# Kernel tuning notes

Measured on AMD Instinct MI355X. Metric: run time of the kernel, lower is better.

## Reference

```python
import jax, jax.numpy as jnp
import numpy as np

B, L, K, D = 4, 48, 32, 128
EPS = 1e-5


def setup_inputs() -> dict:
    key = jax.random.key(0)
    ks = jax.random.split(key, 12)
    s = 1.0 / np.sqrt(D)
    s2 = 1.0 / np.sqrt(2 * D)
    return {
        "h": jax.random.normal(ks[0], (B, L, K, D), jnp.float32),
        # message_mlp: Linear(D,D) -> ReLU -> Linear(D,D); weights stored (in,out)
        "Wm1": jax.random.normal(ks[1], (D, D), jnp.float32) * s,
        "bm1": jnp.zeros((D,), jnp.float32),
        "Wm2": jax.random.normal(ks[2], (D, D), jnp.float32) * s,
        "bm2": jnp.zeros((D,), jnp.float32),
        # attn_mlp: Linear(2D,D) -> ReLU -> Linear(D,1)
        "Wa1": jax.random.normal(ks[3], (2 * D, D), jnp.float32) * s2,
        "ba1": jnp.zeros((D,), jnp.float32),
        "Wa2": jax.random.normal(ks[4], (D, 1), jnp.float32) * s,
        "ba2": jnp.zeros((1,), jnp.float32),
        # LayerNorm(D)
        "gamma": jnp.ones((D,), jnp.float32),
        "beta": jnp.zeros((D,), jnp.float32),
    }


def reference(h, Wm1, bm1, Wm2, bm2, Wa1, ba1, Wa2, ba2, gamma, beta):
    # messages: (B,L,K,D)
    messages = jax.nn.relu(h @ Wm1 + bm1) @ Wm2 + bm2

    # attn_mlp first layer on cat(h_i, h_j): split Wa1 so we never build the 2D concat
    hi_proj = h @ Wa1[:D]   # (B,L,K,D) contribution from h_i (varies over dim 1)
    hj_proj = h @ Wa1[D:]   # (B,L,K,D) contribution from h_j (varies over dim 2)
    # hidden: (B,L,L,K,D)
    hidden = jax.nn.relu(hi_proj[:, :, None, :, :] + hj_proj[:, None, :, :, :] + ba1)
    # logits: (B,L,L,K)
    attn_logits = jnp.einsum("bijkd,d->bijk", hidden, Wa2[:, 0]) + ba2[0]
    attn_weights = jax.nn.softmax(attn_logits, axis=2)  # softmax over j

    # aggregated[b,i,k,:] = sum_j w[b,i,j,k] * messages[b,j,k,:]
    aggregated = jnp.einsum("bijk,bjkd->bikd", attn_weights, messages)

    x = h + aggregated
    mu = jnp.mean(x, axis=-1, keepdims=True)
    var = jnp.mean(jnp.square(x - mu), axis=-1, keepdims=True)
    return (x - mu) * jax.lax.rsqrt(var + EPS) * gamma + beta
```

## Files before the change

### kernel.cpp

```cpp
#include <hip/hip_runtime.h>
#include <math.h>

#define Bc 4
#define Lc 48
#define Kc 32
#define Dc 128
#define ROWS (Bc*Lc*Kc)
#define RT 48
#define NRT (ROWS/RT)
#define GT 512

static_assert(NRT == 128, "role decode assumes 128 row tiles");

__device__ __forceinline__ void gemm_regs(
    const float* __restrict__ sA, const float* __restrict__ sB,
    int rg, int c0, float acc[3][4])
{
    const float* A0 = sA + rg*3*Dc;
    #pragma unroll 8
    for (int k = 0; k < Dc; k += 4) {
        float4 a0 = *(const float4*)(A0 + k);
        float4 a1 = *(const float4*)(A0 + Dc + k);
        float4 a2 = *(const float4*)(A0 + 2*Dc + k);
        float4 b0 = *(const float4*)(sB + (k+0)*Dc + c0);
        float4 b1 = *(const float4*)(sB + (k+1)*Dc + c0);
        float4 b2 = *(const float4*)(sB + (k+2)*Dc + c0);
        float4 b3 = *(const float4*)(sB + (k+3)*Dc + c0);
        float a_[3][4] = {{a0.x,a0.y,a0.z,a0.w},{a1.x,a1.y,a1.z,a1.w},{a2.x,a2.y,a2.z,a2.w}};
        float b_[4][4] = {{b0.x,b0.y,b0.z,b0.w},{b1.x,b1.y,b1.z,b1.w},
                          {b2.x,b2.y,b2.z,b2.w},{b3.x,b3.y,b3.z,b3.w}};
        #pragma unroll
        for (int r = 0; r < 3; ++r)
            #pragma unroll
            for (int c = 0; c < 4; ++c)
                #pragma unroll
                for (int q = 0; q < 4; ++q)
                    acc[r][c] = fmaf(a_[r][q], b_[q][c], acc[r][c]);
    }
}

__global__ __launch_bounds__(GT) void k_gemm_all(
    const float* __restrict__ h,
    const float* __restrict__ Wm1, const float* __restrict__ bm1,
    const float* __restrict__ Wm2, const float* __restrict__ bm2,
    const float* __restrict__ Wa1, const float* __restrict__ ba1,
    float* __restrict__ msg_ws, float* __restrict__ hip_ws,
    float* __restrict__ hjp_ws)
{
    __shared__ float sA[RT*Dc];
    __shared__ float sT[RT*Dc];
    __shared__ float sB[Dc*Dc];
    __shared__ float sBias[Dc];

    const int tid = threadIdx.x;
    const int sel = blockIdx.x >> 7;
    const int r0  = (blockIdx.x & 127) * RT;

    const float* W1; const float* b1;
    if (sel == 0)      { W1 = Wm1;          b1 = bm1; }
    else if (sel == 1) { W1 = Wa1;          b1 = ba1; }
    else               { W1 = Wa1 + Dc*Dc;  b1 = nullptr; }

    {
        const float4* src = (const float4*)W1;
        float4* dst = (float4*)sB;
        #pragma unroll
        for (int i = 0; i < (Dc*Dc/4)/GT; ++i) dst[tid + i*GT] = src[tid + i*GT];
        const float4* asrc = (const float4*)(h + r0*Dc);
        float4* adst = (float4*)sA;
        #pragma unroll
        for (int i = 0; i < (RT*Dc/4)/GT; ++i) adst[tid + i*GT] = asrc[tid + i*GT];
        if (tid < Dc/4)
            ((float4*)sBias)[tid] = b1 ? ((const float4*)b1)[tid]
                                       : make_float4(0.f, 0.f, 0.f, 0.f);
    }
    __syncthreads();

    const int rg = tid >> 5;
    const int c0 = (tid & 31) * 4;
    float acc[3][4] = {};
    gemm_regs(sA, sB, rg, c0, acc);

    if (sel != 0) {
        float* out = (sel == 1) ? hip_ws : hjp_ws;
        #pragma unroll
        for (int r = 0; r < 3; ++r) {
            float4 v;
            v.x = acc[r][0] + sBias[c0+0];
            v.y = acc[r][1] + sBias[c0+1];
            v.z = acc[r][2] + sBias[c0+2];
            v.w = acc[r][3] + sBias[c0+3];
            *(float4*)(out + (r0 + rg*3 + r)*Dc + c0) = v;
        }
        return;
    }

    #pragma unroll
    for (int r = 0; r < 3; ++r) {
        float4 v;
        v.x = fmaxf(acc[r][0] + sBias[c0+0], 0.f);
        v.y = fmaxf(acc[r][1] + sBias[c0+1], 0.f);
        v.z = fmaxf(acc[r][2] + sBias[c0+2], 0.f);
        v.w = fmaxf(acc[r][3] + sBias[c0+3], 0.f);
        *(float4*)(sT + (rg*3+r)*Dc + c0) = v;
    }
    __syncthreads();

    {
        const float4* src = (const float4*)Wm2;
        float4* dst = (float4*)sB;
        #pragma unroll
        for (int i = 0; i < (Dc*Dc/4)/GT; ++i) dst[tid + i*GT] = src[tid + i*GT];
        if (tid < Dc/4) ((float4*)sBias)[tid] = ((const float4*)bm2)[tid];
    }
    __syncthreads();

    float acc2[3][4] = {};
    gemm_regs(sT, sB, rg, c0, acc2);
    #pragma unroll
    for (int r = 0; r < 3; ++r) {
        float4 v;
        v.x = acc2[r][0] + sBias[c0+0];
        v.y = acc2[r][1] + sBias[c0+1];
        v.z = acc2[r][2] + sBias[c0+2];
        v.w = acc2[r][3] + sBias[c0+3];
        *(float4*)(msg_ws + (r0 + rg*3 + r)*Dc + c0) = v;
    }
}

__global__ __launch_bounds__(512) void k_attn(
    const float* __restrict__ h,
    const float* __restrict__ hip_ws, const float* __restrict__ hjp_ws,
    const float* __restrict__ msg_ws,
    const float* __restrict__ wa2, const float* __restrict__ gamma,
    const float* __restrict__ beta, float* __restrict__ out)
{
    const int blk = blockIdx.x;
    const int b  = blk >> 6;
    const int k  = (blk >> 1) & 31;
    const int i0 = (blk & 1) * 24;

    __shared__ float HJ[48*132];
    __shared__ float MS[48*132];
    __shared__ float HI[24*132];
    __shared__ float WA[Dc];
    __shared__ float GM[Dc];
    __shared__ float BT[Dc];
    __shared__ float WT[24*48];

    const int tid = threadIdx.x;

    for (int idx = tid; idx < 48*32; idx += 512) {
        const int j = idx >> 5, c4 = (idx & 31) * 4;
        const int g = ((b*Lc + j)*Kc + k)*Dc + c4;
        *(float4*)(HJ + j*132 + c4) = *(const float4*)(hjp_ws + g);
        *(float4*)(MS + j*132 + c4) = *(const float4*)(msg_ws + g);
    }
    for (int idx = tid; idx < 24*32; idx += 512) {
        const int i = idx >> 5, c4 = (idx & 31) * 4;
        const int g = ((b*Lc + i0 + i)*Kc + k)*Dc + c4;
        *(float4*)(HI + i*132 + c4) = *(const float4*)(hip_ws + g);
    }
    if (tid < 32)       ((float4*)WA)[tid]      = ((const float4*)wa2)[tid];
    else if (tid < 64)  ((float4*)GM)[tid - 32] = ((const float4*)gamma)[tid - 32];
    else if (tid < 96)  ((float4*)BT)[tid - 64] = ((const float4*)beta)[tid - 64];
    __syncthreads();

    const int wave = tid >> 6;
    const int lane = tid & 63;
    const int il0  = wave * 3;
    const bool jv  = lane < 48;
    const int  jl  = jv ? lane : 0;

    float s0 = 0.f, s1 = 0.f, s2 = 0.f;
    {
        const float* hj = HJ + jl*132;
        const float* hA = HI + il0*132;
        const float* hB = hA + 132;
        const float* hC = hB + 132;
        #pragma unroll 4
        for (int d = 0; d < Dc; d += 4) {
            const float4 hj4 = *(const float4*)(hj + d);
            const float4 w4  = *(const float4*)(WA + d);
            const float4 a4  = *(const float4*)(hA + d);
            const float4 b4  = *(const float4*)(hB + d);
            const float4 c4  = *(const float4*)(hC + d);
            s0 = fmaf(fmaxf(a4.x + hj4.x, 0.f), w4.x, s0);
            s0 = fmaf(fmaxf(a4.y + hj4.y, 0.f), w4.y, s0);
            s0 = fmaf(fmaxf(a4.z + hj4.z, 0.f), w4.z, s0);
            s0 = fmaf(fmaxf(a4.w + hj4.w, 0.f), w4.w, s0);
            s1 = fmaf(fmaxf(b4.x + hj4.x, 0.f), w4.x, s1);
            s1 = fmaf(fmaxf(b4.y + hj4.y, 0.f), w4.y, s1);
            s1 = fmaf(fmaxf(b4.z + hj4.z, 0.f), w4.z, s1);
            s1 = fmaf(fmaxf(b4.w + hj4.w, 0.f), w4.w, s1);
            s2 = fmaf(fmaxf(c4.x + hj4.x, 0.f), w4.x, s2);
            s2 = fmaf(fmaxf(c4.y + hj4.y, 0.f), w4.y, s2);
            s2 = fmaf(fmaxf(c4.z + hj4.z, 0.f), w4.z, s2);
            s2 = fmaf(fmaxf(c4.w + hj4.w, 0.f), w4.w, s2);
        }
    }

    float sv[3] = { jv ? s0 : -1e30f, jv ? s1 : -1e30f, jv ? s2 : -1e30f };
    #pragma unroll
    for (int q = 0; q < 3; ++q) {
        float m = sv[q];
        #pragma unroll
        for (int off = 32; off; off >>= 1) m = fmaxf(m, __shfl_xor(m, off));
        const float p = jv ? __expf(sv[q] - m) : 0.f;
        float sum = p;
        #pragma unroll
        for (int off = 32; off; off >>= 1) sum += __shfl_xor(sum, off);
        if (jv) WT[(il0 + q)*48 + lane] = p / sum;
    }
    __syncthreads();

    const int d0 = lane * 2;
    float ac[3][2] = {};
    const float* wt0 = WT + il0*48;
    const float* wt1 = wt0 + 48;
    const float* wt2 = wt1 + 48;
    #pragma unroll 4
    for (int j = 0; j < 48; ++j) {
        const float2 m2 = *(const float2*)(MS + j*132 + d0);
        const float wA = wt0[j], wB = wt1[j], wC = wt2[j];
        ac[0][0] = fmaf(wA, m2.x, ac[0][0]); ac[0][1] = fmaf(wA, m2.y, ac[0][1]);
        ac[1][0] = fmaf(wB, m2.x, ac[1][0]); ac[1][1] = fmaf(wB, m2.y, ac[1][1]);
        ac[2][0] = fmaf(wC, m2.x, ac[2][0]); ac[2][1] = fmaf(wC, m2.y, ac[2][1]);
    }
    const float gm0 = GM[d0], gm1 = GM[d0+1], bt0 = BT[d0], bt1 = BT[d0+1];
    #pragma unroll
    for (int q = 0; q < 3; ++q) {
        const int i = i0 + il0 + q;
        const int g = ((b*Lc + i)*Kc + k)*Dc + d0;
        const float2 h2 = *(const float2*)(h + g);
        const float x0 = h2.x + ac[q][0];
        const float x1 = h2.y + ac[q][1];
        float ps = x0 + x1;
        float pq = x0*x0 + x1*x1;
        #pragma unroll
        for (int off = 32; off; off >>= 1) {
            ps += __shfl_xor(ps, off);
            pq += __shfl_xor(pq, off);
        }
        const float mu  = ps * (1.f/128.f);
        const float var = pq * (1.f/128.f) - mu*mu;
        const float rs  = rsqrtf(var + 1e-5f);
        float2 o2;
        o2.x = (x0 - mu)*rs*gm0 + bt0;
        o2.y = (x1 - mu)*rs*gm1 + bt1;
        *(float2*)(out + g) = o2;
    }
}

extern "C" void kernel_launch(void* const* d_in, const int* in_sizes, int n_in,
                              void* d_out, int out_size, void* d_ws, size_t ws_size,
                              hipStream_t stream)
{
    const float* h     = (const float*)d_in[0];
    const float* Wm1   = (const float*)d_in[1];
    const float* bm1   = (const float*)d_in[2];
    const float* Wm2   = (const float*)d_in[3];
    const float* bm2   = (const float*)d_in[4];
    const float* Wa1   = (const float*)d_in[5];
    const float* ba1   = (const float*)d_in[6];
    const float* wa2   = (const float*)d_in[7];
    const float* gamma = (const float*)d_in[9];
    const float* beta  = (const float*)d_in[10];

    float* msg_ws = (float*)d_ws;
    float* hip_ws = msg_ws + ROWS*Dc;
    float* hjp_ws = hip_ws + ROWS*Dc;
    float* outp   = (float*)d_out;

    hipLaunchKernelGGL(k_gemm_all, dim3(NRT*3),  dim3(GT),  0, stream,
                       h, Wm1, bm1, Wm2, bm2, Wa1, ba1, msg_ws, hip_ws, hjp_ws);
    hipLaunchKernelGGL(k_attn,     dim3(Bc*Kc*2), dim3(512), 0, stream,
                       h, hip_ws, hjp_ws, msg_ws, wa2, gamma, beta, outp);
}
```

Before: 102.4 us.

## Fuse GEMM and attention phases into one cooperative kernel with grid sync

Merges the projection GEMM kernel and the attention/LayerNorm kernel into a single cooperative launch of 256 blocks, separated by a grid-wide barrier, with a shared-memory arena reused by both phases. The attention-projection roles now process 96 rows per block (6x4 register tile) so phase 1 fits the same 256-block grid. This targets the second kernel launch and the inter-kernel gap. The cost is grid-sync overhead and one block per CU. A two-kernel fallback runs if the cooperative launch fails.

Result: slower. 212.9 us (+108.0%).

```diff
diff --git a/kernel.cpp b/kernel.cpp
--- a/kernel.cpp
+++ b/kernel.cpp
@@ -1,18 +1,19 @@
 #include <hip/hip_runtime.h>
+#include <hip/hip_cooperative_groups.h>
 #include <math.h>
+
+namespace cg = cooperative_groups;
 
 #define Bc 4
 #define Lc 48
 #define Kc 32
 #define Dc 128
 #define ROWS (Bc*Lc*Kc)
-#define RT 48
-#define NRT (ROWS/RT)
 #define GT 512
-
-static_assert(NRT == 128, "role decode assumes 128 row tiles");
-
-__device__ __forceinline__ void gemm_regs(
+#define ARENA_F 28800
+
+
+__device__ __forceinline__ void gemm3x4(
     const float* __restrict__ sA, const float* __restrict__ sB,
     int rg, int c0, float acc[3][4])
 {
@@ -39,7 +40,8 @@
     }
 }
 
-__global__ __launch_bounds__(GT) void k_gemm_all(
+__device__ __forceinline__ void phase1(
+    float* arena, int blk, int tid,
     const float* __restrict__ h,
     const float* __restrict__ Wm1, const float* __restrict__ bm1,
     const float* __restrict__ Wm2, const float* __restrict__ bm2,
@@ -47,116 +49,137 @@
     float* __restrict__ msg_ws, float* __restrict__ hip_ws,
     float* __restrict__ hjp_ws)
 {
-    __shared__ float sA[RT*Dc];
-    __shared__ float sT[RT*Dc];
-    __shared__ float sB[Dc*Dc];
-    __shared__ float sBias[Dc];
-
-    const int tid = threadIdx.x;
-    const int sel = blockIdx.x >> 7;
-    const int r0  = (blockIdx.x & 127) * RT;
-
-    const float* W1; const float* b1;
-    if (sel == 0)      { W1 = Wm1;          b1 = bm1; }
-    else if (sel == 1) { W1 = Wa1;          b1 = ba1; }
-    else               { W1 = Wa1 + Dc*Dc;  b1 = nullptr; }
-
-    {
-        const float4* src = (const float4*)W1;
-        float4* dst = (float4*)sB;
-        #pragma unroll
-        for (int i = 0; i < (Dc*Dc/4)/GT; ++i) dst[tid + i*GT] = src[tid + i*GT];
-        const float4* asrc = (const float4*)(h + r0*Dc);
-        float4* adst = (float4*)sA;
-        #pragma unroll
-        for (int i = 0; i < (RT*Dc/4)/GT; ++i) adst[tid + i*GT] = asrc[tid + i*GT];
-        if (tid < Dc/4)
-            ((float4*)sBias)[tid] = b1 ? ((const float4*)b1)[tid]
-                                       : make_float4(0.f, 0.f, 0.f, 0.f);
-    }
-    __syncthreads();
-
+    float* sB    = arena + 12288;
+    float* sBias = arena + 28672;
     const int rg = tid >> 5;
     const int c0 = (tid & 31) * 4;
-    float acc[3][4] = {};
-    gemm_regs(sA, sB, rg, c0, acc);
-
-    if (sel != 0) {
-        float* out = (sel == 1) ? hip_ws : hjp_ws;
+
+    if (blk < 128) {
+        float* sA = arena;
+        float* sT = arena + 6144;
+        const int r0 = blk * 48;
+        {
+            const float4* src = (const float4*)Wm1;
+            float4* dst = (float4*)sB;
+            #pragma unroll
+            for (int i = 0; i < 8; ++i) dst[tid + i*GT] = src[tid + i*GT];
+            const float4* asrc = (const float4*)(h + r0*Dc);
+            float4* adst = (float4*)sA;
+            #pragma unroll
+            for (int i = 0; i < 3; ++i) adst[tid + i*GT] = asrc[tid + i*GT];
+            if (tid < 32) ((float4*)sBias)[tid] = ((const float4*)bm1)[tid];
+        }
+        __syncthreads();
+
+        float acc[3][4] = {};
+        gemm3x4(sA, sB, rg, c0, acc);
         #pragma unroll
         for (int r = 0; r < 3; ++r) {
+            float4 v;
+            v.x = fmaxf(acc[r][0] + sBias[c0+0], 0.f);
+            v.y = fmaxf(acc[r][1] + sBias[c0+1], 0.f);
+            v.z = fmaxf(acc[r][2] + sBias[c0+2], 0.f);
+            v.w = fmaxf(acc[r][3] + sBias[c0+3], 0.f);
+            *(float4*)(sT + (rg*3+r)*Dc + c0) = v;
+        }
+        __syncthreads();
+        {
+            const float4* src = (const float4*)Wm2;
+            float4* dst = (float4*)sB;
+            #pragma unroll
+            for (int i = 0; i < 8; ++i) dst[tid + i*GT] = src[tid + i*GT];
+            if (tid < 32) ((float4*)sBias)[tid] = ((const float4*)bm2)[tid];
+        }
+        __syncthreads();
+
+        float acc2[3][4] = {};
+        gemm3x4(sT, sB, rg, c0, acc2);
+        #pragma unroll
+        for (int r = 0; r < 3; ++r) {
+            float4 v;
+            v.x = acc2[r][0] + sBias[c0+0];
+            v.y = acc2[r][1] + sBias[c0+1];
+            v.z = acc2[r][2] + sBias[c0+2];
+            v.w = acc2[r][3] + sBias[c0+3];
+            *(float4*)(msg_ws + (r0 + rg*3 + r)*Dc + c0) = v;
+        }
+    } else {
+        const bool role1 = blk < 192;
+        const int  r0 = (blk - (role1 ? 128 : 192)) * 96;
+        const float* W = role1 ? Wa1 : (Wa1 + Dc*Dc);
+        float* outp = role1 ? hip_ws : hjp_ws;
+        float* sA = arena;
+        {
+            const float4* src = (const float4*)W;
+            float4* dst = (float4*)sB;
+            #pragma unroll
+            for (int i = 0; i < 8; ++i) dst[tid + i*GT] = src[tid + i*GT];
+            const float4* asrc = (const float4*)(h + r0*Dc);
+            float4* adst = (float4*)sA;
+            #pragma unroll
+            for (int i = 0; i < 6; ++i) adst[tid + i*GT] = asrc[tid + i*GT];
+            if (tid < 32)
+                ((float4*)sBias)[tid] = role1 ? ((const float4*)ba1)[tid]
+                                              : make_float4(0.f, 0.f, 0.f, 0.f);
+        }
+        __syncthreads();
+
+        const float* A0 = sA + rg*6*Dc;
+        float acc[6][4] = {};
+        #pragma unroll 2
+        for (int k = 0; k < Dc; k += 4) {
+            float4 b0 = *(const float4*)(sB + (k+0)*Dc + c0);
+            float4 b1 = *(const float4*)(sB + (k+1)*Dc + c0);
+            float4 b2 = *(const float4*)(sB + (k+2)*Dc + c0);
+            float4 b3 = *(const float4*)(sB + (k+3)*Dc + c0);
+            #pragma unroll
+            for (int r = 0; r < 6; ++r) {
+                float4 a = *(const float4*)(A0 + r*Dc + k);
+                acc[r][0] = fmaf(a.w,b3.x,fmaf(a.z,b2.x,fmaf(a.y,b1.x,fmaf(a.x,b0.x,acc[r][0]))));
+                acc[r][1] = fmaf(a.w,b3.y,fmaf(a.z,b2.y,fmaf(a.y,b1.y,fmaf(a.x,b0.y,acc[r][1]))));
+                acc[r][2] = fmaf(a.w,b3.z,fmaf(a.z,b2.z,fmaf(a.y,b1.z,fmaf(a.x,b0.z,acc[r][2]))));
+                acc[r][3] = fmaf(a.w,b3.w,fmaf(a.z,b2.w,fmaf(a.y,b1.w,fmaf(a.x,b0.w,acc[r][3]))));
+            }
+        }
+        #pragma unroll
+        for (int r = 0; r < 6; ++r) {
             float4 v;
             v.x = acc[r][0] + sBias[c0+0];
             v.y = acc[r][1] + sBias[c0+1];
             v.z = acc[r][2] + sBias[c0+2];
             v.w = acc[r][3] + sBias[c0+3];
-            *(float4*)(out + (r0 + rg*3 + r)*Dc + c0) = v;
-        }
-        return;
-    }
-
-    #pragma unroll
-    for (int r = 0; r < 3; ++r) {
-        float4 v;
-        v.x = fmaxf(acc[r][0] + sBias[c0+0], 0.f);
-        v.y = fmaxf(acc[r][1] + sBias[c0+1], 0.f);
-        v.z = fmaxf(acc[r][2] + sBias[c0+2], 0.f);
-        v.w = fmaxf(acc[r][3] + sBias[c0+3], 0.f);
-        *(float4*)(sT + (rg*3+r)*Dc + c0) = v;
-    }
-    __syncthreads();
-
-    {
-        const float4* src = (const float4*)Wm2;
-        float4* dst = (float4*)sB;
-        #pragma unroll
-        for (int i = 0; i < (Dc*Dc/4)/GT; ++i) dst[tid + i*GT] = src[tid + i*GT];
-        if (tid < Dc/4) ((float4*)sBias)[tid] = ((const float4*)bm2)[tid];
-    }
-    __syncthreads();
-
-    float acc2[3][4] = {};
-    gemm_regs(sT, sB, rg, c0, acc2);
-    #pragma unroll
-    for (int r = 0; r < 3; ++r) {
-        float4 v;
-        v.x = acc2[r][0] + sBias[c0+0];
-        v.y = acc2[r][1] + sBias[c0+1];
-        v.z = acc2[r][2] + sBias[c0+2];
-        v.w = acc2[r][3] + sBias[c0+3];
-        *(float4*)(msg_ws + (r0 + rg*3 + r)*Dc + c0) = v;
-    }
-}
-
-__global__ __launch_bounds__(512) void k_attn(
+            *(float4*)(outp + (r0 + rg*6 + r)*Dc + c0) = v;
+        }
+    }
+}
+
+__device__ __forceinline__ void phase2(
+    float* arena, int blk, int tid,
     const float* __restrict__ h,
     const float* __restrict__ hip_ws, const float* __restrict__ hjp_ws,
     const float* __restrict__ msg_ws,
     const float* __restrict__ wa2, const float* __restrict__ gamma,
     const float* __restrict__ beta, float* __restrict__ out)
 {
-    const int blk = blockIdx.x;
     const int b  = blk >> 6;
     const int k  = (blk >> 1) & 31;
     const int i0 = (blk & 1) * 24;
 
-    __shared__ float HJ[48*132];
-    __shared__ float MS[48*132];
-    __shared__ float HI[24*132];
-    __shared__ float WA[Dc];
-    __shared__ float GM[Dc];
-    __shared__ float BT[Dc];
-    __shared__ float WT[24*48];
-
-    const int tid = threadIdx.x;
-
-    for (int idx = tid; idx < 48*32; idx += 512) {
+    float* HJ = arena;
+    float* MS = arena + 6336;
+    float* HI = arena + 12672;
+    float* WA = arena + 15840;
+    float* GM = arena + 15968;
+    float* BT = arena + 16096;
+    float* WT = arena + 16224;
+
+    for (int idx = tid; idx < 48*32; idx += GT) {
         const int j = idx >> 5, c4 = (idx & 31) * 4;
         const int g = ((b*Lc + j)*Kc + k)*Dc + c4;
         *(float4*)(HJ + j*132 + c4) = *(const float4*)(hjp_ws + g);
         *(float4*)(MS + j*132 + c4) = *(const float4*)(msg_ws + g);
     }
-    for (int idx = tid; idx < 24*32; idx += 512) {
+    for (int idx = tid; idx < 24*32; idx += GT) {
         const int i = idx >> 5, c4 = (idx & 31) * 4;
         const int g = ((b*Lc + i0 + i)*Kc + k)*Dc + c4;
         *(float4*)(HI + i*132 + c4) = *(const float4*)(hip_ws + g);
@@ -252,6 +275,50 @@
     }
 }
 
+__global__ __launch_bounds__(GT, 1) void k_fused(
+    const float* __restrict__ h,
+    const float* __restrict__ Wm1, const float* __restrict__ bm1,
+    const float* __restrict__ Wm2, const float* __restrict__ bm2,
+    const float* __restrict__ Wa1, const float* __restrict__ ba1,
+    const float* __restrict__ wa2, const float* __restrict__ gamma,
+    const float* __restrict__ beta,
+    float* __restrict__ msg_ws, float* __restrict__ hip_ws,
+    float* __restrict__ hjp_ws, float* __restrict__ out)
+{
+    __shared__ float arena[ARENA_F];
+    const int tid = threadIdx.x, blk = blockIdx.x;
+    phase1(arena, blk, tid, h, Wm1, bm1, Wm2, bm2, Wa1, ba1,
+           msg_ws, hip_ws, hjp_ws);
+    __threadfence();
+    cg::this_grid().sync();
+    phase2(arena, blk, tid, h, hip_ws, hjp_ws, msg_ws, wa2, gamma, beta, out);
+}
+
+__global__ __launch_bounds__(GT) void k_p1(
+    const float* __restrict__ h,
+    const float* __restrict__ Wm1, const float* __restrict__ bm1,
+    const float* __restrict__ Wm2, const float* __restrict__ bm2,
+    const float* __restrict__ Wa1, const float* __restrict__ ba1,
+    float* __restrict__ msg_ws, float* __restrict__ hip_ws,
+    float* __restrict__ hjp_ws)
+{
+    __shared__ float arena[ARENA_F];
+    phase1(arena, blockIdx.x, threadIdx.x, h, Wm1, bm1, Wm2, bm2, Wa1, ba1,
+           msg_ws, hip_ws, hjp_ws);
+}
+
+__global__ __launch_bounds__(GT) void k_p2(
+    const float* __restrict__ h,
+    const float* __restrict__ hip_ws, const float* __restrict__ hjp_ws,
+    const float* __restrict__ msg_ws,
+    const float* __restrict__ wa2, const float* __restrict__ gamma,
+    const float* __restrict__ beta, float* __restrict__ out)
+{
+    __shared__ float arena[ARENA_F];
+    phase2(arena, blockIdx.x, threadIdx.x, h, hip_ws, hjp_ws, msg_ws,
+           wa2, gamma, beta, out);
+}
+
 extern "C" void kernel_launch(void* const* d_in, const int* in_sizes, int n_in,
                               void* d_out, int out_size, void* d_ws, size_t ws_size,
                               hipStream_t stream)
@@ -272,8 +339,19 @@
     float* hjp_ws = hip_ws + ROWS*Dc;
     float* outp   = (float*)d_out;
 
-    hipLaunchKernelGGL(k_gemm_all, dim3(NRT*3),  dim3(GT),  0, stream,
-                       h, Wm1, bm1, Wm2, bm2, Wa1, ba1, msg_ws, hip_ws, hjp_ws);
-    hipLaunchKernelGGL(k_attn,     dim3(Bc*Kc*2), dim3(512), 0, stream,
-                       h, hip_ws, hjp_ws, msg_ws, wa2, gamma, beta, outp);
-}
+    void* args[] = { (void*)&h, (void*)&Wm1, (void*)&bm1, (void*)&Wm2,
+                     (void*)&bm2, (void*)&Wa1, (void*)&ba1, (void*)&wa2,
+                     (void*)&gamma, (void*)&beta,
+                     (void*)&msg_ws, (void*)&hip_ws, (void*)&hjp_ws,
+                     (void*)&outp };
+    hipError_t e = hipLaunchCooperativeKernel((const void*)k_fused,
+                                              dim3(256), dim3(GT),
+                                              args, 0, stream);
+    if (e != hipSuccess) {
+        hipLaunchKernelGGL(k_p1, dim3(256), dim3(GT), 0, stream,
+                           h, Wm1, bm1, Wm2, bm2, Wa1, ba1,
+                           msg_ws, hip_ws, hjp_ws);
+        hipLaunchKernelGGL(k_p2, dim3(256), dim3(GT), 0, stream,
+                           h, hip_ws, hjp_ws, msg_ws, wa2, gamma, beta, outp);
+    }
+}
```
